# Kernel optimization log

Measured on AMD Instinct MI355X. Metric: run time of the kernel, lower is better.

## Reference

```python
import jax, jax.numpy as jnp
import numpy as np

EMBED_DIM = 1024
NUM_HEAD = 16
HEAD_DIM = EMBED_DIM // NUM_HEAD
SCALE = HEAD_DIM ** -0.5
EPS = 1e-6


def setup_inputs() -> dict:
    key = jax.random.key(0)
    ks = jax.random.split(key, 8)
    B, N, K, D = 4, 2048, 2048, EMBED_DIM
    x = jax.random.normal(ks[0], (B, N, D), dtype=jnp.float32)
    ctx = jax.random.normal(ks[1], (B, K, D), dtype=jnp.float32)
    w_std = 0.02
    q_w = jax.random.normal(ks[2], (D, D), dtype=jnp.float32) * w_std  # [in, out]
    q_b = jnp.zeros((D,), dtype=jnp.float32)
    kv_w = jax.random.normal(ks[3], (D, 2 * D), dtype=jnp.float32) * w_std
    kv_b = jnp.zeros((2 * D,), dtype=jnp.float32)
    proj_w = jax.random.normal(ks[4], (D, D), dtype=jnp.float32) * w_std
    proj_b = jnp.zeros((D,), dtype=jnp.float32)
    return {"x": x, "ctx": ctx, "q_w": q_w, "q_b": q_b,
            "kv_w": kv_w, "kv_b": kv_b, "proj_w": proj_w, "proj_b": proj_b}


def rms_norm(t):
    return t * jax.lax.rsqrt(jnp.mean(t * t, axis=-1, keepdims=True) + EPS)


def reference(x, ctx, q_w, q_b, kv_w, kv_b, proj_w, proj_b):
    B, N, D = x.shape
    Kc = ctx.shape[1]
    H, Hd = NUM_HEAD, HEAD_DIM
    ctxn = rms_norm(ctx)
    q = (x @ q_w + q_b).reshape(B, N, H, Hd)                 # bnhd
    kv = (ctxn @ kv_w + kv_b).reshape(B, Kc, 2, H, Hd)
    k, v = kv[:, :, 0], kv[:, :, 1]                          # bkhd
    logits = jnp.einsum('bnhd,bkhd->bhnk', q * SCALE, k)
    logits = jnp.clip(logits, -10.0, 10.0)
    attn = jax.nn.softmax(logits, axis=-1)                   # bhnk
    out = jnp.einsum('bhnk,bkhd->bnhd', attn, v).reshape(B, N, D)
    out = out @ proj_w + proj_b
    return out, attn.mean()
```

## Files before the change

### kernel.cpp

```cpp
#include <hip/hip_runtime.h>
#include <hip/hip_bf16.h>
#include <stdint.h>


typedef __bf16 bf16_t;
typedef __bf16 bf16x8 __attribute__((ext_vector_type(8)));
typedef __bf16 bf16x4 __attribute__((ext_vector_type(4)));
typedef float  f32x4  __attribute__((ext_vector_type(4)));

#define BB 4
#define NN 2048
#define KC 2048
#define DD 1024
#define NH 16
#define HD 64
#define QSCALE 0.18033688011112042f
#define CLIP2  14.426950408889634f

__device__ __forceinline__ f32x4 mfma_16x16x32(bf16x8 a, bf16x8 b, f32x4 c) {
  return __builtin_amdgcn_mfma_f32_16x16x32_bf16(a, b, c, 0, 0, 0);
}

__device__ __forceinline__ void gl_lds16(const bf16_t* g, bf16_t* l) {
  __builtin_amdgcn_global_load_lds(
      (const __attribute__((address_space(1))) void*)g,
      (__attribute__((address_space(3))) void*)l, 16, 0, 0);
}

__global__ __launch_bounds__(256) void cvt_f32_bf16(const float* __restrict__ in,
                                                    bf16_t* __restrict__ out, int n4) {
  int i = blockIdx.x * 256 + threadIdx.x;
  if (i >= n4) return;
  float4 v = ((const float4*)in)[i];
  bf16x4 o = {(bf16_t)v.x, (bf16_t)v.y, (bf16_t)v.z, (bf16_t)v.w};
  ((bf16x4*)out)[i] = o;
}

__global__ __launch_bounds__(256) void rmsnorm_rows(const float* __restrict__ in,
                                                    bf16_t* __restrict__ out) {
  int row = blockIdx.x, tid = threadIdx.x;
  float4 v = ((const float4*)(in + (size_t)row * DD))[tid];
  float ss = v.x * v.x + v.y * v.y + v.z * v.z + v.w * v.w;
#pragma unroll
  for (int m = 1; m < 64; m <<= 1) ss += __shfl_xor(ss, m);
  __shared__ float wsum[4];
  if ((tid & 63) == 0) wsum[tid >> 6] = ss;
  __syncthreads();
  float total = wsum[0] + wsum[1] + wsum[2] + wsum[3];
  float scale = rsqrtf(total * (1.0f / (float)DD) + 1e-6f);
  bf16x4 o = {(bf16_t)(v.x * scale), (bf16_t)(v.y * scale),
              (bf16_t)(v.z * scale), (bf16_t)(v.w * scale)};
  ((bf16x4*)(out + (size_t)row * DD))[tid] = o;
}

__global__ __launch_bounds__(256) void transpose_w(const float* __restrict__ W,
                                                   bf16_t* __restrict__ WT, int R, int C) {
  __shared__ float tile[32][33];
  int tx = threadIdx.x & 31, ty = threadIdx.x >> 5;
  int r0 = blockIdx.y * 32, c0 = blockIdx.x * 32;
#pragma unroll
  for (int i = 0; i < 4; i++) tile[ty + 8 * i][tx] = W[(size_t)(r0 + ty + 8 * i) * C + c0 + tx];
  __syncthreads();
#pragma unroll
  for (int i = 0; i < 4; i++)
    WT[(size_t)(c0 + ty + 8 * i) * R + r0 + tx] = (bf16_t)tile[tx][ty + 8 * i];
}

template <int MODE>
__global__ __launch_bounds__(256, 2) void gemm_bt(const bf16_t* __restrict__ A,
                                                  const bf16_t* __restrict__ Bt,
                                                  const float* __restrict__ bias,
                                                  void* __restrict__ Cout,
                                                  bf16_t* __restrict__ kP,
                                                  bf16_t* __restrict__ vP, int M, int N,
                                                  int Kd, float alpha, int gxlog) {
  __shared__ bf16_t As[128 * 32];
  __shared__ bf16_t Bs[128 * 32];
  int tid = threadIdx.x;
  int w = tid >> 6, lane = tid & 63;
  int quad = lane >> 4, l16 = lane & 15;
  int bid = blockIdx.x;
  int xcd = bid & 7, idx = bid >> 3;
  int row0 = (xcd * 8 + (idx >> gxlog)) * 128;
  int col0 = (idx & ((1 << gxlog) - 1)) * 128;
  int wm = (w >> 1) * 64, wn = (w & 1) * 64;

  f32x4 acc[4][4];
#pragma unroll
  for (int i = 0; i < 4; i++)
#pragma unroll
    for (int j = 0; j < 4; j++) acc[i][j] = (f32x4){0.f, 0.f, 0.f, 0.f};

  for (int kk = 0; kk < Kd; kk += 32) {
#pragma unroll
    for (int call = 0; call < 2; call++) {
      int c = w * 128 + call * 64 + lane;
      gl_lds16(&A[(size_t)(row0 + (c >> 2)) * Kd + kk + (c & 3) * 8],
               &As[(w * 128 + call * 64) * 8]);
      gl_lds16(&Bt[(size_t)(col0 + (c >> 2)) * Kd + kk + (c & 3) * 8],
               &Bs[(w * 128 + call * 64) * 8]);
    }
    __syncthreads();
    bf16x8 af[4], bfr[4];
#pragma unroll
    for (int mi = 0; mi < 4; mi++)
      af[mi] = *(const bf16x8*)&As[(wm + mi * 16 + l16) * 32 + quad * 8];
#pragma unroll
    for (int ni = 0; ni < 4; ni++)
      bfr[ni] = *(const bf16x8*)&Bs[(wn + ni * 16 + l16) * 32 + quad * 8];
#pragma unroll
    for (int mi = 0; mi < 4; mi++)
#pragma unroll
      for (int ni = 0; ni < 4; ni++) acc[mi][ni] = mfma_16x16x32(af[mi], bfr[ni], acc[mi][ni]);
    __syncthreads();
  }

  if (MODE == 2) {
    bool isK = (col0 < 1024);
    int cpart[4];
    float bv[4];
#pragma unroll
    for (int ni = 0; ni < 4; ni++) {
      int col = col0 + wn + ni * 16 + l16;
      bv[ni] = bias[col];
      int ch = isK ? col : (col - 1024);
      int h = ch >> 6, hd = ch & 63;
      if (isK)
        cpart[ni] = h * 131072 + (hd >> 5) * 512 + ((hd >> 3) & 3) * 8 + (hd & 7);
      else
        cpart[ni] = h * 131072 + (hd >> 4) * 512 + (hd & 15) * 32;
    }
#pragma unroll
    for (int mi = 0; mi < 4; mi++) {
#pragma unroll
      for (int r = 0; r < 4; r++) {
        int row = row0 + wm + mi * 16 + quad * 4 + r;
        int bb = row >> 11, kc = row & 2047;
        int t = kc >> 6, key = kc & 63;
        int rpart;
        if (isK) {
          rpart = bb * 2097152 + t * 4096 + (key >> 4) * 1024 + (key & 15) * 32;
        } else {
          int g = key >> 5, k2 = key & 31;
          rpart = bb * 2097152 + t * 4096 + g * 2048 + ((k2 >> 2) & 3) * 8 +
                  (((k2 >> 4) << 2) | (k2 & 3));
        }
        bf16_t* dst = isK ? kP : vP;
#pragma unroll
        for (int ni = 0; ni < 4; ni++)
          dst[(size_t)rpart + cpart[ni]] = (bf16_t)((acc[mi][ni][r] + bv[ni]) * alpha);
      }
    }
    return;
  }

#pragma unroll
  for (int ni = 0; ni < 4; ni++) {
    int col = col0 + wn + ni * 16 + l16;
    float bv = bias[col];
#pragma unroll
    for (int mi = 0; mi < 4; mi++) {
#pragma unroll
      for (int r = 0; r < 4; r++) {
        int row = row0 + wm + mi * 16 + quad * 4 + r;
        float v = (acc[mi][ni][r] + bv) * alpha;
        if (MODE == 1)
          ((float*)Cout)[(size_t)row * N + col] = v;
        else
          ((bf16_t*)Cout)[(size_t)row * N + col] = (bf16_t)v;
      }
    }
  }
}

__global__ __launch_bounds__(128, 2) void flash_attn(const bf16_t* __restrict__ qbuf,
                                                     const bf16_t* __restrict__ kP,
                                                     const bf16_t* __restrict__ vP,
                                                     bf16_t* __restrict__ attn_out) {
  __shared__ bf16_t Kp[4096];
  __shared__ bf16_t Vp[4096];
  __shared__ float rsinvS[2][64];

  int tid = threadIdx.x, w = tid >> 6, lane = tid & 63;
  int quad = lane >> 4, l16 = lane & 15;
  int bid = blockIdx.x;
  int xcd = bid & 7, slot = bid >> 3;
  int bh = xcd * 8 + (slot >> 4);
  int qt = slot & 15;
  int b = bh >> 4, h = bh & 15;
  int n0 = qt * 128 + w * 64;

  const bf16_t* kpb = kP + (size_t)bh * 32 * 4096;
  const bf16_t* vpb = vP + (size_t)bh * 32 * 4096;

  bf16x8 qf[4][2];
#pragma unroll
  for (int qi = 0; qi < 4; qi++)
#pragma unroll
    for (int dc = 0; dc < 2; dc++)
      qf[qi][dc] = *(const bf16x8*)&qbuf[((size_t)b * NN + n0 + qi * 16 + l16) * DD + h * HD +
                                         dc * 32 + quad * 8];

  f32x4 o[4][4];
#pragma unroll
  for (int qi = 0; qi < 4; qi++)
#pragma unroll
    for (int hb = 0; hb < 4; hb++) o[qi][hb] = (f32x4){0.f, 0.f, 0.f, 0.f};
  float rs[4] = {0.f, 0.f, 0.f, 0.f};

  for (int t = 0; t < KC / 64; t++) {
    __syncthreads();
#pragma unroll
    for (int i = 0; i < 4; i++) {
      int j = w * 4 + i;
      gl_lds16(&kpb[(size_t)t * 4096 + j * 512 + lane * 8], &Kp[j * 512]);
      gl_lds16(&vpb[(size_t)t * 4096 + j * 512 + lane * 8], &Vp[j * 512]);
    }
    __syncthreads();

    bf16x8 kf[4][2];
#pragma unroll
    for (int ki = 0; ki < 4; ki++)
#pragma unroll
      for (int dc = 0; dc < 2; dc++)
        kf[ki][dc] = *(const bf16x8*)&Kp[(ki * 2 + dc) * 512 + (l16 * 4 + quad) * 8];
    bf16x8 vb[2][4];
#pragma unroll
    for (int g = 0; g < 2; g++)
#pragma unroll
      for (int hb = 0; hb < 4; hb++)
        vb[g][hb] = *(const bf16x8*)&Vp[(g * 4 + hb) * 512 + (l16 * 4 + quad) * 8];

#pragma unroll
    for (int qi = 0; qi < 4; qi++) {
#pragma unroll
      for (int g = 0; g < 2; g++) {
        union { bf16x8 v8; bf16x4 h[2]; } pf;
#pragma unroll
        for (int sub = 0; sub < 2; sub++) {
          f32x4 s = (f32x4){0.f, 0.f, 0.f, 0.f};
          s = mfma_16x16x32(kf[g * 2 + sub][0], qf[qi][0], s);
          s = mfma_16x16x32(kf[g * 2 + sub][1], qf[qi][1], s);
          bf16x4 pb;
#pragma unroll
          for (int r = 0; r < 4; r++) {
            float pv = __builtin_amdgcn_exp2f(__builtin_amdgcn_fmed3f(s[r], -CLIP2, CLIP2));
            rs[qi] += pv;
            pb[r] = (bf16_t)pv;
          }
          pf.h[sub] = pb;
        }
#pragma unroll
        for (int hb = 0; hb < 4; hb++)
          o[qi][hb] = mfma_16x16x32(pf.v8, vb[g][hb], o[qi][hb]);
      }
    }
  }

#pragma unroll
  for (int qi = 0; qi < 4; qi++) {
    float v = rs[qi];
    v += __shfl_xor(v, 16);
    v += __shfl_xor(v, 32);
    if (quad == 0) rsinvS[w][qi * 16 + l16] = 1.0f / v;
  }
#pragma unroll
  for (int qi = 0; qi < 4; qi++) {
    f32x4 ri = *(const f32x4*)&rsinvS[w][qi * 16 + quad * 4];
#pragma unroll
    for (int hb = 0; hb < 4; hb++) {
#pragma unroll
      for (int r = 0; r < 4; r++) {
        int row = n0 + qi * 16 + quad * 4 + r;
        int col = h * HD + hb * 16 + l16;
        attn_out[((size_t)b * NN + row) * DD + col] = (bf16_t)(o[qi][hb][r] * ri[r]);
      }
    }
  }
}

__global__ void write_mean(float* out) { out[0] = 1.0f / 2048.0f; }

extern "C" void kernel_launch(void* const* d_in, const int* in_sizes, int n_in, void* d_out,
                              int out_size, void* d_ws, size_t ws_size, hipStream_t stream) {
  const float* x      = (const float*)d_in[0];
  const float* ctx    = (const float*)d_in[1];
  const float* q_w    = (const float*)d_in[2];
  const float* q_b    = (const float*)d_in[3];
  const float* kv_w   = (const float*)d_in[4];
  const float* kv_b   = (const float*)d_in[5];
  const float* proj_w = (const float*)d_in[6];
  const float* proj_b = (const float*)d_in[7];
  float* out = (float*)d_out;
  char* ws = (char*)d_ws;

  bf16_t* xb    = (bf16_t*)(ws + 0);
  bf16_t* ctxn  = (bf16_t*)(ws + 16777216);
  bf16_t* qwT   = (bf16_t*)(ws + 33554432);
  bf16_t* kvwT  = (bf16_t*)(ws + 35651584);
  bf16_t* pwT   = (bf16_t*)(ws + 39845888);
  bf16_t* qbuf  = (bf16_t*)(ws + 41943040);
  bf16_t* kP    = (bf16_t*)(ws + 58720256);
  bf16_t* vP    = (bf16_t*)(ws + 75497472);
  bf16_t* attn_out = xb;

  cvt_f32_bf16<<<8192, 256, 0, stream>>>(x, xb, (BB * NN * DD) / 4);
  rmsnorm_rows<<<BB * KC, 256, 0, stream>>>(ctx, ctxn);
  transpose_w<<<dim3(32, 32), 256, 0, stream>>>(q_w, qwT, DD, DD);
  transpose_w<<<dim3(64, 32), 256, 0, stream>>>(kv_w, kvwT, DD, 2 * DD);
  transpose_w<<<dim3(32, 32), 256, 0, stream>>>(proj_w, pwT, DD, DD);
  gemm_bt<0><<<512, 256, 0, stream>>>(xb, qwT, q_b, qbuf, nullptr, nullptr,
                                      BB * NN, DD, DD, QSCALE, 3);
  gemm_bt<2><<<1024, 256, 0, stream>>>(ctxn, kvwT, kv_b, nullptr, kP, vP,
                                       BB * KC, 2 * DD, DD, 1.0f, 4);
  flash_attn<<<1024, 128, 0, stream>>>(qbuf, kP, vP, attn_out);
  gemm_bt<1><<<512, 256, 0, stream>>>(attn_out, pwT, proj_b, out, nullptr, nullptr,
                                      BB * NN, DD, DD, 1.0f, 3);
  write_mean<<<1, 1, 0, stream>>>(out + (size_t)out_size - 1);
}
```

Baseline: 335.8 us.

## Merge prep and QKV GEMM launches, fold mean write, double-tile flash attention

Combines the bf16 conversion, RMSNorm and weight transposes into a single block-indexed prep kernel, and the Q and KV projections into one GEMM launch. The constant mean output is written from the projection GEMM instead of a separate kernel. Flash attention now loads two K/V tiles per barrier pair, halving synchronisation at the cost of doubled LDS per block. The aim is less launch overhead and better tail utilisation, with some risk of reduced occupancy in attention.

```diff
diff --git a/kernel.cpp b/kernel.cpp
--- a/kernel.cpp
+++ b/kernel.cpp
@@ -27,37 +27,10 @@
       (__attribute__((address_space(3))) void*)l, 16, 0, 0);
 }
 
-__global__ __launch_bounds__(256) void cvt_f32_bf16(const float* __restrict__ in,
-                                                    bf16_t* __restrict__ out, int n4) {
-  int i = blockIdx.x * 256 + threadIdx.x;
-  if (i >= n4) return;
-  float4 v = ((const float4*)in)[i];
-  bf16x4 o = {(bf16_t)v.x, (bf16_t)v.y, (bf16_t)v.z, (bf16_t)v.w};
-  ((bf16x4*)out)[i] = o;
-}
-
-__global__ __launch_bounds__(256) void rmsnorm_rows(const float* __restrict__ in,
-                                                    bf16_t* __restrict__ out) {
-  int row = blockIdx.x, tid = threadIdx.x;
-  float4 v = ((const float4*)(in + (size_t)row * DD))[tid];
-  float ss = v.x * v.x + v.y * v.y + v.z * v.z + v.w * v.w;
-#pragma unroll
-  for (int m = 1; m < 64; m <<= 1) ss += __shfl_xor(ss, m);
-  __shared__ float wsum[4];
-  if ((tid & 63) == 0) wsum[tid >> 6] = ss;
-  __syncthreads();
-  float total = wsum[0] + wsum[1] + wsum[2] + wsum[3];
-  float scale = rsqrtf(total * (1.0f / (float)DD) + 1e-6f);
-  bf16x4 o = {(bf16_t)(v.x * scale), (bf16_t)(v.y * scale),
-              (bf16_t)(v.z * scale), (bf16_t)(v.w * scale)};
-  ((bf16x4*)(out + (size_t)row * DD))[tid] = o;
-}
-
-__global__ __launch_bounds__(256) void transpose_w(const float* __restrict__ W,
-                                                   bf16_t* __restrict__ WT, int R, int C) {
-  __shared__ float tile[32][33];
-  int tx = threadIdx.x & 31, ty = threadIdx.x >> 5;
-  int r0 = blockIdx.y * 32, c0 = blockIdx.x * 32;
+__device__ __forceinline__ void transpose_tile(const float* W, bf16_t* WT, int R, int C,
+                                               int bx, int by, int tid, float (*tile)[33]) {
+  int tx = tid & 31, ty = tid >> 5;
+  int r0 = by * 32, c0 = bx * 32;
 #pragma unroll
   for (int i = 0; i < 4; i++) tile[ty + 8 * i][tx] = W[(size_t)(r0 + ty + 8 * i) * C + c0 + tx];
   __syncthreads();
@@ -66,20 +39,56 @@
     WT[(size_t)(c0 + ty + 8 * i) * R + r0 + tx] = (bf16_t)tile[tx][ty + 8 * i];
 }
 
+__global__ __launch_bounds__(256) void prep(const float* __restrict__ x,
+                                            const float* __restrict__ ctx,
+                                            const float* __restrict__ q_w,
+                                            const float* __restrict__ kv_w,
+                                            const float* __restrict__ proj_w,
+                                            bf16_t* __restrict__ xb, bf16_t* __restrict__ ctxn,
+                                            bf16_t* __restrict__ qwT, bf16_t* __restrict__ kvwT,
+                                            bf16_t* __restrict__ pwT) {
+  __shared__ float tile[32][33];
+  int bid = blockIdx.x, tid = threadIdx.x;
+  if (bid < 8192) {
+    int i = bid * 256 + tid;
+    float4 v = ((const float4*)x)[i];
+    bf16x4 o = {(bf16_t)v.x, (bf16_t)v.y, (bf16_t)v.z, (bf16_t)v.w};
+    ((bf16x4*)xb)[i] = o;
+  } else if (bid < 16384) {
+    int row = bid - 8192;
+    float4 v = ((const float4*)(ctx + (size_t)row * DD))[tid];
+    float ss = v.x * v.x + v.y * v.y + v.z * v.z + v.w * v.w;
+#pragma unroll
+    for (int m = 1; m < 64; m <<= 1) ss += __shfl_xor(ss, m);
+    if ((tid & 63) == 0) tile[0][tid >> 6] = ss;
+    __syncthreads();
+    float total = tile[0][0] + tile[0][1] + tile[0][2] + tile[0][3];
+    float scale = rsqrtf(total * (1.0f / (float)DD) + 1e-6f);
+    bf16x4 o = {(bf16_t)(v.x * scale), (bf16_t)(v.y * scale),
+                (bf16_t)(v.z * scale), (bf16_t)(v.w * scale)};
+    ((bf16x4*)(ctxn + (size_t)row * DD))[tid] = o;
+  } else if (bid < 17408) {
+    int idx = bid - 16384;
+    transpose_tile(q_w, qwT, DD, DD, idx & 31, idx >> 5, tid, tile);
+  } else if (bid < 19456) {
+    int idx = bid - 17408;
+    transpose_tile(kv_w, kvwT, DD, 2 * DD, idx & 63, idx >> 6, tid, tile);
+  } else {
+    int idx = bid - 19456;
+    transpose_tile(proj_w, pwT, DD, DD, idx & 31, idx >> 5, tid, tile);
+  }
+}
+
 template <int MODE>
-__global__ __launch_bounds__(256, 2) void gemm_bt(const bf16_t* __restrict__ A,
-                                                  const bf16_t* __restrict__ Bt,
-                                                  const float* __restrict__ bias,
-                                                  void* __restrict__ Cout,
-                                                  bf16_t* __restrict__ kP,
-                                                  bf16_t* __restrict__ vP, int M, int N,
-                                                  int Kd, float alpha, int gxlog) {
-  __shared__ bf16_t As[128 * 32];
-  __shared__ bf16_t Bs[128 * 32];
+__device__ __forceinline__ void gemm_core(const bf16_t* __restrict__ A,
+                                          const bf16_t* __restrict__ Bt,
+                                          const float* __restrict__ bias,
+                                          void* __restrict__ Cout, bf16_t* __restrict__ kP,
+                                          bf16_t* __restrict__ vP, int N, int Kd, float alpha,
+                                          int gxlog, int bid, bf16_t* As, bf16_t* Bs) {
   int tid = threadIdx.x;
   int w = tid >> 6, lane = tid & 63;
   int quad = lane >> 4, l16 = lane & 15;
-  int bid = blockIdx.x;
   int xcd = bid & 7, idx = bid >> 3;
   int row0 = (xcd * 8 + (idx >> gxlog)) * 128;
   int col0 = (idx & ((1 << gxlog) - 1)) * 128;
@@ -157,7 +166,8 @@
 #pragma unroll
   for (int ni = 0; ni < 4; ni++) {
     int col = col0 + wn + ni * 16 + l16;
-    float bv = bias[col];
+    float bv = bias[ni == 0 ? col : col];
+    bv = bias[col];
 #pragma unroll
     for (int mi = 0; mi < 4; mi++) {
 #pragma unroll
@@ -173,12 +183,41 @@
   }
 }
 
+__global__ __launch_bounds__(256, 2) void gemm_qkv(const bf16_t* __restrict__ xb,
+                                                   const bf16_t* __restrict__ qwT,
+                                                   const float* __restrict__ q_b,
+                                                   bf16_t* __restrict__ qbuf,
+                                                   const bf16_t* __restrict__ ctxn,
+                                                   const bf16_t* __restrict__ kvwT,
+                                                   const float* __restrict__ kv_b,
+                                                   bf16_t* __restrict__ kP,
+                                                   bf16_t* __restrict__ vP) {
+  __shared__ bf16_t As[128 * 32];
+  __shared__ bf16_t Bs[128 * 32];
+  int bid = blockIdx.x;
+  if (bid < 512)
+    gemm_core<0>(xb, qwT, q_b, qbuf, nullptr, nullptr, DD, DD, QSCALE, 3, bid, As, Bs);
+  else
+    gemm_core<2>(ctxn, kvwT, kv_b, nullptr, kP, vP, 2 * DD, DD, 1.0f, 4, bid - 512, As, Bs);
+}
+
+__global__ __launch_bounds__(256, 2) void gemm_proj(const bf16_t* __restrict__ attn_out,
+                                                    const bf16_t* __restrict__ pwT,
+                                                    const float* __restrict__ proj_b,
+                                                    float* __restrict__ out) {
+  __shared__ bf16_t As[128 * 32];
+  __shared__ bf16_t Bs[128 * 32];
+  gemm_core<1>(attn_out, pwT, proj_b, out, nullptr, nullptr, DD, DD, 1.0f, 3, blockIdx.x, As, Bs);
+  if (blockIdx.x == 0 && threadIdx.x == 0)
+    out[(size_t)BB * NN * DD] = 1.0f / 2048.0f;
+}
+
 __global__ __launch_bounds__(128, 2) void flash_attn(const bf16_t* __restrict__ qbuf,
                                                      const bf16_t* __restrict__ kP,
                                                      const bf16_t* __restrict__ vP,
                                                      bf16_t* __restrict__ attn_out) {
-  __shared__ bf16_t Kp[4096];
-  __shared__ bf16_t Vp[4096];
+  __shared__ bf16_t Kp[2][4096];
+  __shared__ bf16_t Vp[2][4096];
   __shared__ float rsinvS[2][64];
 
   int tid = threadIdx.x, w = tid >> 6, lane = tid & 63;
@@ -208,51 +247,57 @@
     for (int hb = 0; hb < 4; hb++) o[qi][hb] = (f32x4){0.f, 0.f, 0.f, 0.f};
   float rs[4] = {0.f, 0.f, 0.f, 0.f};
 
-  for (int t = 0; t < KC / 64; t++) {
-    __syncthreads();
-#pragma unroll
-    for (int i = 0; i < 4; i++) {
-      int j = w * 4 + i;
-      gl_lds16(&kpb[(size_t)t * 4096 + j * 512 + lane * 8], &Kp[j * 512]);
-      gl_lds16(&vpb[(size_t)t * 4096 + j * 512 + lane * 8], &Vp[j * 512]);
-    }
-    __syncthreads();
-
-    bf16x8 kf[4][2];
-#pragma unroll
-    for (int ki = 0; ki < 4; ki++)
-#pragma unroll
-      for (int dc = 0; dc < 2; dc++)
-        kf[ki][dc] = *(const bf16x8*)&Kp[(ki * 2 + dc) * 512 + (l16 * 4 + quad) * 8];
-    bf16x8 vb[2][4];
-#pragma unroll
-    for (int g = 0; g < 2; g++)
-#pragma unroll
-      for (int hb = 0; hb < 4; hb++)
-        vb[g][hb] = *(const bf16x8*)&Vp[(g * 4 + hb) * 512 + (l16 * 4 + quad) * 8];
-
-#pragma unroll
-    for (int qi = 0; qi < 4; qi++) {
-#pragma unroll
-      for (int g = 0; g < 2; g++) {
-        union { bf16x8 v8; bf16x4 h[2]; } pf;
-#pragma unroll
-        for (int sub = 0; sub < 2; sub++) {
-          f32x4 s = (f32x4){0.f, 0.f, 0.f, 0.f};
-          s = mfma_16x16x32(kf[g * 2 + sub][0], qf[qi][0], s);
-          s = mfma_16x16x32(kf[g * 2 + sub][1], qf[qi][1], s);
-          bf16x4 pb;
-#pragma unroll
-          for (int r = 0; r < 4; r++) {
-            float pv = __builtin_amdgcn_exp2f(__builtin_amdgcn_fmed3f(s[r], -CLIP2, CLIP2));
-            rs[qi] += pv;
-            pb[r] = (bf16_t)pv;
+  for (int t = 0; t < KC / 64; t += 2) {
+    __syncthreads();
+#pragma unroll
+    for (int u = 0; u < 2; u++) {
+#pragma unroll
+      for (int i = 0; i < 4; i++) {
+        int j = w * 4 + i;
+        gl_lds16(&kpb[(size_t)(t + u) * 4096 + j * 512 + lane * 8], &Kp[u][j * 512]);
+        gl_lds16(&vpb[(size_t)(t + u) * 4096 + j * 512 + lane * 8], &Vp[u][j * 512]);
+      }
+    }
+    __syncthreads();
+
+#pragma unroll
+    for (int u = 0; u < 2; u++) {
+      bf16x8 kf[4][2];
+#pragma unroll
+      for (int ki = 0; ki < 4; ki++)
+#pragma unroll
+        for (int dc = 0; dc < 2; dc++)
+          kf[ki][dc] = *(const bf16x8*)&Kp[u][(ki * 2 + dc) * 512 + (l16 * 4 + quad) * 8];
+      bf16x8 vb[2][4];
+#pragma unroll
+      for (int g = 0; g < 2; g++)
+#pragma unroll
+        for (int hb = 0; hb < 4; hb++)
+          vb[g][hb] = *(const bf16x8*)&Vp[u][(g * 4 + hb) * 512 + (l16 * 4 + quad) * 8];
+
+#pragma unroll
+      for (int qi = 0; qi < 4; qi++) {
+#pragma unroll
+        for (int g = 0; g < 2; g++) {
+          union { bf16x8 v8; bf16x4 h[2]; } pf;
+#pragma unroll
+          for (int sub = 0; sub < 2; sub++) {
+            f32x4 s = (f32x4){0.f, 0.f, 0.f, 0.f};
+            s = mfma_16x16x32(kf[g * 2 + sub][0], qf[qi][0], s);
+            s = mfma_16x16x32(kf[g * 2 + sub][1], qf[qi][1], s);
+            bf16x4 pb;
+#pragma unroll
+            for (int r = 0; r < 4; r++) {
+              float pv = __builtin_amdgcn_exp2f(__builtin_amdgcn_fmed3f(s[r], -CLIP2, CLIP2));
+              rs[qi] += pv;
+              pb[r] = (bf16_t)pv;
+            }
+            pf.h[sub] = pb;
           }
-          pf.h[sub] = pb;
+#pragma unroll
+          for (int hb = 0; hb < 4; hb++)
+            o[qi][hb] = mfma_16x16x32(pf.v8, vb[g][hb], o[qi][hb]);
         }
-#pragma unroll
-        for (int hb = 0; hb < 4; hb++)
-          o[qi][hb] = mfma_16x16x32(pf.v8, vb[g][hb], o[qi][hb]);
       }
     }
   }
@@ -278,8 +323,6 @@
     }
   }
 }
-
-__global__ void write_mean(float* out) { out[0] = 1.0f / 2048.0f; }
 
 extern "C" void kernel_launch(void* const* d_in, const int* in_sizes, int n_in, void* d_out,
                               int out_size, void* d_ws, size_t ws_size, hipStream_t stream) {
@@ -304,17 +347,8 @@
   bf16_t* vP    = (bf16_t*)(ws + 75497472);
   bf16_t* attn_out = xb;
 
-  cvt_f32_bf16<<<8192, 256, 0, stream>>>(x, xb, (BB * NN * DD) / 4);
-  rmsnorm_rows<<<BB * KC, 256, 0, stream>>>(ctx, ctxn);
-  transpose_w<<<dim3(32, 32), 256, 0, stream>>>(q_w, qwT, DD, DD);
-  transpose_w<<<dim3(64, 32), 256, 0, stream>>>(kv_w, kvwT, DD, 2 * DD);
-  transpose_w<<<dim3(32, 32), 256, 0, stream>>>(proj_w, pwT, DD, DD);
-  gemm_bt<0><<<512, 256, 0, stream>>>(xb, qwT, q_b, qbuf, nullptr, nullptr,
-                                      BB * NN, DD, DD, QSCALE, 3);
-  gemm_bt<2><<<1024, 256, 0, stream>>>(ctxn, kvwT, kv_b, nullptr, kP, vP,
-                                       BB * KC, 2 * DD, DD, 1.0f, 4);
+  prep<<<20480, 256, 0, stream>>>(x, ctx, q_w, kv_w, proj_w, xb, ctxn, qwT, kvwT, pwT);
+  gemm_qkv<<<1536, 256, 0, stream>>>(xb, qwT, q_b, qbuf, ctxn, kvwT, kv_b, kP, vP);
   flash_attn<<<1024, 128, 0, stream>>>(qbuf, kP, vP, attn_out);
-  gemm_bt<1><<<512, 256, 0, stream>>>(attn_out, pwT, proj_b, out, nullptr, nullptr,
-                                      BB * NN, DD, DD, 1.0f, 3);
-  write_mean<<<1, 1, 0, stream>>>(out + (size_t)out_size - 1);
-}
+  gemm_proj<<<512, 256, 0, stream>>>(attn_out, pwT, proj_b, out);
+}
```

Result: slower. 349.3 us (+4.0%).
